# Kernel optimization log

Measured on AMD Instinct MI355X. Metric: run time of the kernel, lower is better.

Reference implementation:

```python
import jax, jax.numpy as jnp
import numpy as np

C = 1.0          # curvature
TOP_K = 5
LAMBDA_H = 0.01
TAU = 0.1        # forward default
NEG_SAMPLES = 20 # forward default
EPS = 1e-9
B, D = 4096, 64


def _to_ball(v):
    # map gaussian vectors strictly inside the unit Poincare ball
    return 0.8 * v / (1.0 + jnp.linalg.norm(v, axis=-1, keepdims=True))


def setup_inputs() -> dict:
    key = jax.random.key(0)
    ka, kt = jax.random.split(key)
    audio = _to_ball(jax.random.normal(ka, (B, D), dtype=jnp.float32))
    text = _to_ball(jax.random.normal(kt, (B, D), dtype=jnp.float32))
    return {"audio_embeds": audio, "text_embeds": text}


def _pairwise_poincare(x, y, c=C):
    # ||x-y||^2 via gemm instead of materializing [N,N,D] diff tensor
    x_sq = jnp.sum(x * x, axis=-1, keepdims=True)          # [N,1]
    y_sq = jnp.sum(y * y, axis=-1, keepdims=True).T        # [1,M]
    diff_sq = jnp.maximum(x_sq + y_sq - 2.0 * (x @ y.T), 0.0)
    x_cl = jnp.minimum(x_sq, 1.0 - EPS)
    y_cl = jnp.minimum(y_sq, 1.0 - EPS)
    denom = jnp.maximum((1.0 - x_cl) * (1.0 - y_cl), EPS)
    z = jnp.maximum(1.0 + 2.0 * diff_sq / denom, 1.0 + EPS)
    return jnp.arccosh(z) / jnp.sqrt(jnp.asarray(c, x.dtype))


def _topk_triplet(embeds, key):
    n = embeds.shape[0]
    dist = _pairwise_poincare(embeds, embeds)
    dist = dist.at[jnp.arange(n), jnp.arange(n)].set(jnp.inf)  # fill_diagonal_(inf)
    k = min(TOP_K, n - 1)
    neg_pos, pos_idx = jax.lax.top_k(-dist, k)                 # k smallest distances
    pos_term = jax.scipy.special.logsumexp(neg_pos / TAU, axis=1)  # logsumexp(-pos_dist/tau)
    # mask out top-k positives (diagonal stays in pool, holding +inf -> exp(-inf)=0)
    mask = jnp.ones((n, n), bool).at[jnp.arange(n)[:, None], pos_idx].set(False)
    # stable argsort: mask-True columns first, in original column order -> matches dist[i][mask[i]]
    order = jnp.argsort(jnp.where(mask, 0, 1), axis=1)
    pool = jnp.take_along_axis(dist, order[:, : n - k], axis=1)    # [n, n-k]
    samp = jax.random.randint(key, (n, NEG_SAMPLES), 0, n - k)
    neg_vals = jnp.take_along_axis(pool, samp, axis=1)             # [n, NEG_SAMPLES]
    neg_term = jax.scipy.special.logsumexp(-neg_vals / TAU, axis=1)
    return jnp.mean(neg_term - pos_term)  # mean of -(pos_term - neg_term)


def reference(audio_embeds, text_embeds):
    # HyperbolicLayeredLoss.forward returns lambda_h * (text_h + audio_h);
    # the cross-modal loss is computed but NOT added to the returned total in the source.
    key_text = jax.random.key(1)
    key_audio = jax.random.key(2)
    loss_text_h = _topk_triplet(text_embeds, key_text)
    loss_audio_h = _topk_triplet(audio_embeds, key_audio)
    return LAMBDA_H * (loss_text_h + loss_audio_h)
```

## Files before the change

kernel.cpp:

```cpp
#include <hip/hip_runtime.h>
#include <stdint.h>

#define JAX_PARTITIONABLE 1

constexpr int N = 4096;
constexpr int DIM = 64;
constexpr int TOPK = 5;
constexpr int NEGS = 20;
constexpr float TAU_ = 0.1f;
constexpr uint32_t SPAN = 4091u;
constexpr uint32_t MULT = 2309u;

constexpr int CQ = 256;
constexpr int NQ = N / CQ;
constexpr int NT = CQ / 16;
constexpr int RPB = 64;
constexpr int YSTRIDE = 136;

typedef __attribute__((ext_vector_type(8))) short bf16x8;
typedef __attribute__((ext_vector_type(4))) float f32x4;

__device__ __forceinline__ uint32_t rotl32(uint32_t v, int d) {
  return (v << d) | (v >> (32 - d));
}

__device__ __forceinline__ void threefry(uint32_t k0, uint32_t k1,
                                         uint32_t& x0, uint32_t& x1) {
  const uint32_t k2 = k0 ^ k1 ^ 0x1BD11BDAu;
  x0 += k0; x1 += k1;
#define TF_R(r) { x0 += x1; x1 = rotl32(x1, r); x1 ^= x0; }
  TF_R(13) TF_R(15) TF_R(26) TF_R(6)
  x0 += k1; x1 += k2 + 1u;
  TF_R(17) TF_R(29) TF_R(16) TF_R(24)
  x0 += k2; x1 += k0 + 2u;
  TF_R(13) TF_R(15) TF_R(26) TF_R(6)
  x0 += k0; x1 += k1 + 3u;
  TF_R(17) TF_R(29) TF_R(16) TF_R(24)
  x0 += k1; x1 += k2 + 4u;
  TF_R(13) TF_R(15) TF_R(26) TF_R(6)
  x0 += k2; x1 += k0 + 5u;
#undef TF_R
}

__device__ __forceinline__ uint32_t sample_idx(uint32_t seed, uint32_t f) {
#if JAX_PARTITIONABLE
  uint32_t a0 = 0u, a1 = 0u; threefry(0u, seed, a0, a1);
  uint32_t b0 = 0u, b1 = 1u; threefry(0u, seed, b0, b1);
  uint32_t h0 = 0u, h1 = f;  threefry(a0, a1, h0, h1);
  const uint32_t hi = h0 ^ h1;
  uint32_t l0 = 0u, l1 = f;  threefry(b0, b1, l0, l1);
  const uint32_t lo = l0 ^ l1;
#else
  uint32_t a0 = 0u, a1 = 2u; threefry(0u, seed, a0, a1);
  uint32_t c0 = 1u, c1 = 3u; threefry(0u, seed, c0, c1);
  const uint32_t HALF = (uint32_t)(N * NEGS / 2);
  uint32_t hi, lo;
  if (f < HALF) {
    uint32_t x0 = f, x1 = f + HALF; threefry(a0, c0, x0, x1); hi = x0;
    x0 = f; x1 = f + HALF;          threefry(a1, c1, x0, x1); lo = x0;
  } else {
    uint32_t x0 = f - HALF, x1 = f; threefry(a0, c0, x0, x1); hi = x1;
    x0 = f - HALF; x1 = f;          threefry(a1, c1, x0, x1); lo = x1;
  }
#endif
  return ((hi % SPAN) * MULT + (lo % SPAN)) % SPAN;
}

__device__ __forceinline__ float acosh_dev(float z) {
  return logf(z + sqrtf((z - 1.0f) * (z + 1.0f)));
}

__device__ __forceinline__ uint16_t f2bf(float f) {
  const uint32_t u = __float_as_uint(f);
  return (uint16_t)((u + 0x7FFFu + ((u >> 16) & 1u)) >> 16);
}
__device__ __forceinline__ float bf2f(uint16_t h) {
  return __uint_as_float((uint32_t)h << 16);
}

__global__ __launch_bounds__(64) void k_pre(const float* __restrict__ Xa,
                                            const float* __restrict__ Xt,
                                            uint16_t* __restrict__ Xs,
                                            float* __restrict__ ysq,
                                            float* __restrict__ inv) {
  const int m = blockIdx.y;
  const float* __restrict__ X = (m == 0) ? Xt : Xa;
  const int i = blockIdx.x * 64 + threadIdx.x;
  const float* xr = X + (size_t)i * DIM;

  uint32_t hb[DIM / 2], lb[DIM / 2];
  float s = 0.0f;
#pragma unroll
  for (int u = 0; u < DIM / 4; ++u) {
    const float4 v = *(const float4*)(xr + 4 * u);
    s = fmaf(v.x, v.x, s); s = fmaf(v.y, v.y, s);
    s = fmaf(v.z, v.z, s); s = fmaf(v.w, v.w, s);
    const uint16_t h0 = f2bf(v.x), h1 = f2bf(v.y), h2 = f2bf(v.z), h3 = f2bf(v.w);
    const uint16_t l0 = f2bf(v.x - bf2f(h0)), l1 = f2bf(v.y - bf2f(h1));
    const uint16_t l2 = f2bf(v.z - bf2f(h2)), l3 = f2bf(v.w - bf2f(h3));
    hb[2 * u]     = (uint32_t)h0 | ((uint32_t)h1 << 16);
    hb[2 * u + 1] = (uint32_t)h2 | ((uint32_t)h3 << 16);
    lb[2 * u]     = (uint32_t)l0 | ((uint32_t)l1 << 16);
    lb[2 * u + 1] = (uint32_t)l2 | ((uint32_t)l3 << 16);
  }
  uint32_t* dst = (uint32_t*)(Xs + (size_t)(m * N + i) * 128);
#pragma unroll
  for (int w = 0; w < 8; ++w) {
    uint4 qh = { hb[4 * w], hb[4 * w + 1], hb[4 * w + 2], hb[4 * w + 3] };
    ((uint4*)dst)[w] = qh;
  }
#pragma unroll
  for (int w = 0; w < 8; ++w) {
    uint4 ql = { lb[4 * w], lb[4 * w + 1], lb[4 * w + 2], lb[4 * w + 3] };
    ((uint4*)dst)[8 + w] = ql;
  }
  ysq[m * N + i] = s;
  inv[m * N + i] = 1.0f / (1.0f - fminf(s, 1.0f));
}

__global__ __launch_bounds__(256) void k_top5(
    const uint16_t* __restrict__ Xs, const float* __restrict__ ysq,
    const float* __restrict__ inv, uint64_t* __restrict__ partial) {
  const int lin = (int)blockIdx.x;
  const int wg = ((lin & 7) << 8) | (lin >> 3);
  const int m = wg >> 10;
  const int qq = (wg >> 6) & 15;
  const int rb = wg & 63;

  const int tid = (int)threadIdx.x;
  const int wid = tid >> 6;
  const int l = tid & 63;
  const int i0w = rb * RPB + wid * 16;
  const int j0q = qq * CQ;
  const int mN = m * N;
  const uint16_t* __restrict__ Xm = Xs + (size_t)m * N * 128;
  const int lc = l & 15;
  const int lk = l >> 4;
  const int lk4 = lk * 4;
  const int lk8 = lk * 8;
  const int sr = tid >> 4;
  const int sc8 = (tid & 15) * 8;

  __shared__ __align__(16) unsigned char smem[4 * 16 * YSTRIDE * 2 + 2048];
  uint16_t* ybuf = (uint16_t*)smem;
  float* sq_s = (float*)(smem + 4 * 16 * YSTRIDE * 2);
  float* iv_s = sq_s + CQ;

  bf16x8 xf[2][2];
#pragma unroll
  for (int c = 0; c < 2; ++c)
#pragma unroll
    for (int h = 0; h < 2; ++h)
      xf[c][h] = *(const bf16x8*)(Xm + (size_t)(i0w + lc) * 128 +
                                  h * 64 + c * 32 + lk8);

  const float xsq_i = ysq[mN + i0w + lc];
  const float inv2_i = 2.0f * inv[mN + i0w + lc];
  const int gi = i0w + lc;

  const uint64_t SENT = ((uint64_t)0x7F800000u << 32) | 0xFFFFFFFFu;
  uint64_t t5[TOPK];
#pragma unroll
  for (int t = 0; t < TOPK; ++t) t5[t] = SENT;
  float z5own = __uint_as_float(0x7F800000u);

  const f32x4 zz = {0.0f, 0.0f, 0.0f, 0.0f};
  const float INF_ = __uint_as_float(0x7F800000u);

  {
    if (tid < 64)
      *(float4*)&sq_s[tid * 4] = *(const float4*)&ysq[mN + j0q + tid * 4];
    else if (tid < 128)
      *(float4*)&iv_s[(tid - 64) * 4] =
          *(const float4*)&inv[mN + j0q + (tid - 64) * 4];
    *(uint4*)(ybuf + sr * YSTRIDE + sc8) =
        *(const uint4*)(Xm + (size_t)(j0q + sr) * 128 + sc8);
    *(uint4*)(ybuf + 16 * YSTRIDE + sr * YSTRIDE + sc8) =
        *(const uint4*)(Xm + (size_t)(j0q + 16 + sr) * 128 + sc8);
    __syncthreads();
  }

#define PROCESS(T, BUF)                                                        \
  {                                                                            \
    const uint16_t* yp = (BUF) + lc * YSTRIDE + lk8;                           \
    const bf16x8 Y0 = *(const bf16x8*)(yp);                                    \
    const bf16x8 Y1 = *(const bf16x8*)(yp + 32);                               \
    const bf16x8 Y2 = *(const bf16x8*)(yp + 64);                               \
    const bf16x8 Y3 = *(const bf16x8*)(yp + 96);                               \
    f32x4 acc;                \
    acc = __builtin_amdgcn_mfma_f32_16x16x32_bf16(Y0, xf[0][0], zz, 0, 0, 0);  \
    acc = __builtin_amdgcn_mfma_f32_16x16x32_bf16(Y1, xf[1][0], acc, 0, 0, 0); \
    acc = __builtin_amdgcn_mfma_f32_16x16x32_bf16(Y2, xf[0][0], acc, 0, 0, 0); \
    acc = __builtin_amdgcn_mfma_f32_16x16x32_bf16(Y3, xf[1][0], acc, 0, 0, 0); \
    acc = __builtin_amdgcn_mfma_f32_16x16x32_bf16(Y0, xf[0][1], acc, 0, 0, 0); \
    acc = __builtin_amdgcn_mfma_f32_16x16x32_bf16(Y1, xf[1][1], acc, 0, 0, 0); \
    const float4 sq4 = *(const float4*)&sq_s[(T) * 16 + lk4];                  \
    const float4 iv4 = *(const float4*)&iv_s[(T) * 16 + lk4];                  \
    const int jb = j0q + (T) * 16;                                             \
    float zt[4];                                                               \
    _Pragma("unroll") for (int p = 0; p < 4; ++p) {                            \
      const float yc = (p == 0) ? sq4.x : (p == 1) ? sq4.y                     \
                      : (p == 2) ? sq4.z : sq4.w;                              \
      const float ic = (p == 0) ? iv4.x : (p == 1) ? iv4.y                     \
                      : (p == 2) ? iv4.z : iv4.w;                              \
      const float diff = fmaxf(xsq_i + yc - 2.0f * acc[p], 0.0f);              \
      zt[p] = fmaf(diff * inv2_i, ic, 1.0f);                                   \
    }                                                                          \
    if (jb == i0w) {                           \
      _Pragma("unroll") for (int p = 0; p < 4; ++p)                            \
        if (gi == jb + lk4 + p) zt[p] = INF_;                                  \
    }                                                                          \
    const float zm = fminf(fminf(zt[0], zt[1]), fminf(zt[2], zt[3]));          \
    if (zm <= z5own) {                                                         \
      _Pragma("unroll") for (int p = 0; p < 4; ++p) {                          \
        uint64_t key = ((uint64_t)__float_as_uint(zt[p]) << 32) |              \
                       (uint32_t)(jb + lk4 + p);                               \
        if (key < t5[TOPK - 1]) {                                              \
          _Pragma("unroll") for (int tt = 0; tt < TOPK; ++tt) {                \
            const uint64_t cv = t5[tt];                                        \
            if (key < cv) { t5[tt] = key; key = cv; }                          \
          }                                                                    \
        }                                                                      \
      }                                                                        \
      z5own = __uint_as_float((uint32_t)(t5[TOPK - 1] >> 32));                 \
    }                                                                          \
  }

#pragma unroll 1
  for (int T = 0; T < NT; T += 2) {
    const bool hn = (T + 2 < NT);
    uint4 s2, s3;
    if (hn) {
      s2 = *(const uint4*)(Xm + (size_t)(j0q + (T + 2) * 16 + sr) * 128 + sc8);
      s3 = *(const uint4*)(Xm + (size_t)(j0q + (T + 3) * 16 + sr) * 128 + sc8);
    }
    PROCESS(T, ybuf + (size_t)((T) & 3) * 16 * YSTRIDE)
    PROCESS(T + 1, ybuf + (size_t)((T + 1) & 3) * 16 * YSTRIDE)
    if (hn) {
      *(uint4*)(ybuf + (size_t)((T + 2) & 3) * 16 * YSTRIDE + sr * YSTRIDE + sc8) = s2;
      *(uint4*)(ybuf + (size_t)((T + 3) & 3) * 16 * YSTRIDE + sr * YSTRIDE + sc8) = s3;
    }
    __syncthreads();
  }
#undef PROCESS

  uint64_t* mb = (uint64_t*)smem;
#pragma unroll
  for (int t = 0; t < TOPK; ++t)
    mb[((size_t)(wid * 16) + lc) * 21 + lk * TOPK + t] = t5[t];
  __syncthreads();

  if (l < 16) {
    uint64_t cur[TOPK];
#pragma unroll
    for (int t = 0; t < TOPK; ++t) cur[t] = mb[((size_t)(wid * 16) + l) * 21 + t];
    for (int c = 1; c < 4; ++c) {
      for (int t = 0; t < TOPK; ++t) {
        uint64_t key = mb[((size_t)(wid * 16) + l) * 21 + c * TOPK + t];
        if (key >= cur[TOPK - 1]) break;
#pragma unroll
        for (int u = 0; u < TOPK; ++u) {
          const uint64_t cv = cur[u];
          if (key < cv) { cur[u] = key; key = cv; }
        }
      }
    }
#pragma unroll
    for (int t = 0; t < TOPK; ++t)
      partial[((size_t)(m * NQ + qq) * N + i0w + l) * TOPK + t] = cur[t];
  }
}

__global__ __launch_bounds__(64) void k_neg(const float* __restrict__ Xa,
                                            const float* __restrict__ Xt,
                                            const float* __restrict__ ysq,
                                            const float* __restrict__ inv,
                                            const uint64_t* __restrict__ partial,
                                            float* __restrict__ rowres) {
  const int m = blockIdx.y;
  const int i = blockIdx.x;
  const float* __restrict__ X = (m == 0) ? Xt : Xa;
  const uint32_t seed = (m == 0) ? 1u : 2u;
  const int lane = threadIdx.x;

  __shared__ float4 xi4[DIM / 4];
  __shared__ float posv[TOPK];
  if (lane < DIM / 4) xi4[lane] = ((const float4*)(X + (size_t)i * DIM))[lane];
  __syncthreads();

  uint64_t cur[TOPK];
#pragma unroll
  for (int t = 0; t < TOPK; ++t)
    cur[t] = partial[((size_t)(m * NQ) * N + i) * TOPK + t];
  for (int q = 1; q < NQ; ++q) {
    for (int t = 0; t < TOPK; ++t) {
      uint64_t key = partial[((size_t)(m * NQ + q) * N + i) * TOPK + t];
      if (key >= cur[TOPK - 1]) break;
#pragma unroll
      for (int u = 0; u < TOPK; ++u) {
        const uint64_t cv = cur[u];
        if (key < cv) { cur[u] = key; key = cv; }
      }
    }
  }

  const float ysq_i = ysq[m * N + i];
  const float inv_i = inv[m * N + i];

  if (lane >= 32 && lane < 32 + TOPK) {
    const int t = lane - 32;
    const uint32_t c = (uint32_t)(cur[t] & 0xffffffffu);
    const float4* xc = (const float4*)(X + (size_t)c * DIM);
    float dot = 0.0f;
#pragma unroll
    for (int k = 0; k < DIM / 4; ++k) {
      const float4 a = xi4[k];
      const float4 b = xc[k];
      dot = fmaf(a.x, b.x, dot); dot = fmaf(a.y, b.y, dot);
      dot = fmaf(a.z, b.z, dot); dot = fmaf(a.w, b.w, dot);
    }
    const float diff = fmaxf(ysq_i + ysq[m * N + c] - 2.0f * dot, 0.0f);
    const float z = 1.0f + 2.0f * diff * inv_i * inv[m * N + c];
    posv[t] = -acosh_dev(z) / TAU_;
  }

  uint32_t pidx[TOPK];
#pragma unroll
  for (int t = 0; t < TOPK; ++t) pidx[t] = (uint32_t)(cur[t] & 0xffffffffu);

#define CSWAP(a, b)                                                           \
  { const uint32_t mn = pidx[a] < pidx[b] ? pidx[a] : pidx[b];                \
    const uint32_t mx = pidx[a] < pidx[b] ? pidx[b] : pidx[a];                \
    pidx[a] = mn; pidx[b] = mx; }
  CSWAP(0, 1) CSWAP(3, 4) CSWAP(2, 4) CSWAP(2, 3) CSWAP(1, 4)
  CSWAP(0, 3) CSWAP(0, 2) CSWAP(1, 3) CSWAP(1, 2)
#undef CSWAP

  float v = -1e30f;
  if (lane < NEGS) {
    const uint32_t f = (uint32_t)i * (uint32_t)NEGS + (uint32_t)lane;
    uint32_t c = sample_idx(seed, f);
#pragma unroll
    for (int t = 0; t < TOPK; ++t) c += (c >= pidx[t]) ? 1u : 0u;
    if (c != (uint32_t)i) {
      const float4* xc = (const float4*)(X + (size_t)c * DIM);
      float dot = 0.0f;
#pragma unroll
      for (int k = 0; k < DIM / 4; ++k) {
        const float4 a = xi4[k];
        const float4 b = xc[k];
        dot = fmaf(a.x, b.x, dot); dot = fmaf(a.y, b.y, dot);
        dot = fmaf(a.z, b.z, dot); dot = fmaf(a.w, b.w, dot);
      }
      const float diff = fmaxf(ysq_i + ysq[m * N + c] - 2.0f * dot, 0.0f);
      const float z = 1.0f + 2.0f * diff * inv_i * inv[m * N + c];
      v = -acosh_dev(z) / TAU_;
    }
  }

  __syncthreads();

  float vmax = v;
#pragma unroll
  for (int o = 32; o > 0; o >>= 1) vmax = fmaxf(vmax, __shfl_xor(vmax, o, 64));
  float e = expf(v - vmax);
  float ss = e;
#pragma unroll
  for (int o = 32; o > 0; o >>= 1) ss += __shfl_xor(ss, o, 64);

  if (lane == 0) {
    float vm = -1e30f;
#pragma unroll
    for (int t = 0; t < TOPK; ++t) vm = fmaxf(vm, posv[t]);
    float ps = 0.0f;
#pragma unroll
    for (int t = 0; t < TOPK; ++t) ps += expf(posv[t] - vm);
    const float pos = vm + logf(ps);
    rowres[m * N + i] = (vmax + logf(ss)) - pos;
  }
}

__global__ __launch_bounds__(256) void k_reduce(const float* __restrict__ rowres,
                                                float* __restrict__ out) {
  __shared__ double sh[256];
  double s = 0.0;
  for (int idx = threadIdx.x; idx < 2 * N; idx += 256) s += (double)rowres[idx];
  sh[threadIdx.x] = s;
  __syncthreads();
  for (int o = 128; o > 0; o >>= 1) {
    if (threadIdx.x < o) sh[threadIdx.x] += sh[threadIdx.x + o];
    __syncthreads();
  }
  if (threadIdx.x == 0) out[0] = (float)(0.01 * (sh[0] / (double)N));
}

extern "C" void kernel_launch(void* const* d_in, const int* in_sizes, int n_in,
                              void* d_out, int out_size, void* d_ws,
                              size_t ws_size, hipStream_t stream) {
  const float* Xa = (const float*)d_in[0];
  const float* Xt = (const float*)d_in[1];
  float* out = (float*)d_out;

  float* ysq = (float*)d_ws;
  float* inv = ysq + 2 * N;
  uint64_t* partial = (uint64_t*)(inv + 2 * N);
  float* rowres = (float*)(partial + (size_t)2 * NQ * N * TOPK);
  uint16_t* Xs = (uint16_t*)(rowres + 2 * N);

  k_pre<<<dim3(N / 64, 2), 64, 0, stream>>>(Xa, Xt, Xs, ysq, inv);
  k_top5<<<(N / RPB) * NQ * 2, 256, 0, stream>>>(Xs, ysq, inv, partial);
  k_neg<<<dim3(N, 2), 64, 0, stream>>>(Xa, Xt, ysq, inv, partial, rowres);
  k_reduce<<<1, 256, 0, stream>>>(rowres, out);
}
```

Measured before the change: 104.8 us.

## Split top-5 search into bound pass and filtered scan with candidate lists

The full top-5 pass over all 16 column chunks is replaced by two stages. A bound kernel computes a top-5 over 4 of the chunks, and a scan kernel goes over the other 12 chunks. The scan only appends keys that beat the 5th-best bound to a per-row list, using atomics, instead of keeping a sorted insertion per tile. k_neg then merges the partial results with the list. This cuts the in-loop top-5 maintenance and the partial traffic, but adds a launch, atomics, and a CAP=64 overflow risk that could drop true neighbours.

Result: faster. 100.1 us, median of 2 (-4.6%).

```diff
diff --git a/kernel.cpp b/kernel.cpp
--- a/kernel.cpp
+++ b/kernel.cpp
@@ -12,10 +12,11 @@
 constexpr uint32_t MULT = 2309u;
 
 constexpr int CQ = 256;
-constexpr int NQ = N / CQ;
 constexpr int NT = CQ / 16;
 constexpr int RPB = 64;
 constexpr int YSTRIDE = 136;
+constexpr int NQB = 4;
+constexpr int CAP = 64;
 
 typedef __attribute__((ext_vector_type(8))) short bf16x8;
 typedef __attribute__((ext_vector_type(4))) float f32x4;
@@ -82,7 +83,8 @@
                                             const float* __restrict__ Xt,
                                             uint16_t* __restrict__ Xs,
                                             float* __restrict__ ysq,
-                                            float* __restrict__ inv) {
+                                            float* __restrict__ inv,
+                                            uint32_t* __restrict__ cnt) {
   const int m = blockIdx.y;
   const float* __restrict__ X = (m == 0) ? Xt : Xa;
   const int i = blockIdx.x * 64 + threadIdx.x;
@@ -116,22 +118,22 @@
   }
   ysq[m * N + i] = s;
   inv[m * N + i] = 1.0f / (1.0f - fminf(s, 1.0f));
-}
-
-__global__ __launch_bounds__(256) void k_top5(
+  cnt[m * N + i] = 0u;
+}
+
+__global__ __launch_bounds__(256) void k_bound(
     const uint16_t* __restrict__ Xs, const float* __restrict__ ysq,
     const float* __restrict__ inv, uint64_t* __restrict__ partial) {
-  const int lin = (int)blockIdx.x;
-  const int wg = ((lin & 7) << 8) | (lin >> 3);
-  const int m = wg >> 10;
-  const int qq = (wg >> 6) & 15;
-  const int rb = wg & 63;
+  const int rb = (int)blockIdx.x;
+  const int qs = (int)blockIdx.y;
+  const int m = (int)blockIdx.z;
+  const int qr = rb >> 4;
+  const int j0q = (qr * NQB + qs) * CQ;
 
   const int tid = (int)threadIdx.x;
   const int wid = tid >> 6;
   const int l = tid & 63;
   const int i0w = rb * RPB + wid * 16;
-  const int j0q = qq * CQ;
   const int mN = m * N;
   const uint16_t* __restrict__ Xm = Xs + (size_t)m * N * 128;
   const int lc = l & 15;
@@ -206,7 +208,7 @@
       const float diff = fmaxf(xsq_i + yc - 2.0f * acc[p], 0.0f);              \
       zt[p] = fmaf(diff * inv2_i, ic, 1.0f);                                   \
     }                                                                          \
-    if (jb == i0w) {                           \
+    if (jb == i0w) {                                                           \
       _Pragma("unroll") for (int p = 0; p < 4; ++p)                            \
         if (gi == jb + lk4 + p) zt[p] = INF_;                                  \
     }                                                                          \
@@ -267,8 +269,140 @@
     }
 #pragma unroll
     for (int t = 0; t < TOPK; ++t)
-      partial[((size_t)(m * NQ + qq) * N + i0w + l) * TOPK + t] = cur[t];
-  }
+      partial[((size_t)(m * NQB + qs) * N + i0w + l) * TOPK + t] = cur[t];
+  }
+}
+
+__global__ __launch_bounds__(256) void k_scan(
+    const uint16_t* __restrict__ Xs, const float* __restrict__ ysq,
+    const float* __restrict__ inv, const uint64_t* __restrict__ partial,
+    uint32_t* __restrict__ cnt, uint64_t* __restrict__ rowlist) {
+  const int rb = (int)blockIdx.x;
+  const int s = (int)blockIdx.y;
+  const int m = (int)blockIdx.z;
+  const int qr = rb >> 4;
+  const int gs = (s < qr * NQB) ? s : s + NQB;
+  const int j0q = gs * CQ;
+
+  const int tid = (int)threadIdx.x;
+  const int wid = tid >> 6;
+  const int l = tid & 63;
+  const int i0w = rb * RPB + wid * 16;
+  const int mN = m * N;
+  const uint16_t* __restrict__ Xm = Xs + (size_t)m * N * 128;
+  const int lc = l & 15;
+  const int lk = l >> 4;
+  const int lk4 = lk * 4;
+  const int lk8 = lk * 8;
+  const int sr = tid >> 4;
+  const int sc8 = (tid & 15) * 8;
+  const int gi = i0w + lc;
+
+  __shared__ __align__(16) unsigned char smem[4 * 16 * YSTRIDE * 2 + 2048];
+  uint16_t* ybuf = (uint16_t*)smem;
+  float* sq_s = (float*)(smem + 4 * 16 * YSTRIDE * 2);
+  float* iv_s = sq_s + CQ;
+
+  bf16x8 xf[2][2];
+#pragma unroll
+  for (int c = 0; c < 2; ++c)
+#pragma unroll
+    for (int h = 0; h < 2; ++h)
+      xf[c][h] = *(const bf16x8*)(Xm + (size_t)gi * 128 + h * 64 + c * 32 + lk8);
+
+  const float xsq_i = ysq[mN + gi];
+  const float inv2_i = 2.0f * inv[mN + gi];
+
+  uint64_t b5[TOPK];
+#pragma unroll
+  for (int t = 0; t < TOPK; ++t)
+    b5[t] = partial[((size_t)(m * NQB) * N + gi) * TOPK + t];
+  for (int q = 1; q < NQB; ++q) {
+    for (int t = 0; t < TOPK; ++t) {
+      uint64_t key = partial[((size_t)(m * NQB + q) * N + gi) * TOPK + t];
+      if (key >= b5[TOPK - 1]) break;
+#pragma unroll
+      for (int u = 0; u < TOPK; ++u) {
+        const uint64_t cv = b5[u];
+        if (key < cv) { b5[u] = key; key = cv; }
+      }
+    }
+  }
+  const uint64_t bound = b5[TOPK - 1];
+  const float bz = __uint_as_float((uint32_t)(bound >> 32));
+
+  const f32x4 zz = {0.0f, 0.0f, 0.0f, 0.0f};
+
+  {
+    if (tid < 64)
+      *(float4*)&sq_s[tid * 4] = *(const float4*)&ysq[mN + j0q + tid * 4];
+    else if (tid < 128)
+      *(float4*)&iv_s[(tid - 64) * 4] =
+          *(const float4*)&inv[mN + j0q + (tid - 64) * 4];
+    *(uint4*)(ybuf + sr * YSTRIDE + sc8) =
+        *(const uint4*)(Xm + (size_t)(j0q + sr) * 128 + sc8);
+    *(uint4*)(ybuf + 16 * YSTRIDE + sr * YSTRIDE + sc8) =
+        *(const uint4*)(Xm + (size_t)(j0q + 16 + sr) * 128 + sc8);
+    __syncthreads();
+  }
+
+#define PSCAN(T, BUF)                                                          \
+  {                                                                            \
+    const uint16_t* yp = (BUF) + lc * YSTRIDE + lk8;                           \
+    const bf16x8 Y0 = *(const bf16x8*)(yp);                                    \
+    const bf16x8 Y1 = *(const bf16x8*)(yp + 32);                               \
+    const bf16x8 Y2 = *(const bf16x8*)(yp + 64);                               \
+    const bf16x8 Y3 = *(const bf16x8*)(yp + 96);                               \
+    f32x4 acc;                        \
+    acc = __builtin_amdgcn_mfma_f32_16x16x32_bf16(Y0, xf[0][0], zz, 0, 0, 0);  \
+    acc = __builtin_amdgcn_mfma_f32_16x16x32_bf16(Y1, xf[1][0], acc, 0, 0, 0); \
+    acc = __builtin_amdgcn_mfma_f32_16x16x32_bf16(Y2, xf[0][0], acc, 0, 0, 0); \
+    acc = __builtin_amdgcn_mfma_f32_16x16x32_bf16(Y3, xf[1][0], acc, 0, 0, 0); \
+    acc = __builtin_amdgcn_mfma_f32_16x16x32_bf16(Y0, xf[0][1], acc, 0, 0, 0); \
+    acc = __builtin_amdgcn_mfma_f32_16x16x32_bf16(Y1, xf[1][1], acc, 0, 0, 0); \
+    const float4 sq4 = *(const float4*)&sq_s[(T) * 16 + lk4];                  \
+    const float4 iv4 = *(const float4*)&iv_s[(T) * 16 + lk4];                  \
+    const int jb = j0q + (T) * 16;                                             \
+    float zt[4];                                                               \
+    _Pragma("unroll") for (int p = 0; p < 4; ++p) {                            \
+      const float yc = (p == 0) ? sq4.x : (p == 1) ? sq4.y                     \
+                      : (p == 2) ? sq4.z : sq4.w;                              \
+      const float ic = (p == 0) ? iv4.x : (p == 1) ? iv4.y                     \
+                      : (p == 2) ? iv4.z : iv4.w;                              \
+      const float diff = fmaxf(xsq_i + yc - 2.0f * acc[p], 0.0f);              \
+      zt[p] = fmaf(diff * inv2_i, ic, 1.0f);                                   \
+    }                                                                          \
+    const float zm = fminf(fminf(zt[0], zt[1]), fminf(zt[2], zt[3]));          \
+    if (zm <= bz) {                   \
+      _Pragma("unroll") for (int p = 0; p < 4; ++p) {                          \
+        const uint64_t key = ((uint64_t)__float_as_uint(zt[p]) << 32) |        \
+                             (uint32_t)(jb + lk4 + p);                         \
+        if (key < bound) {                                                     \
+          const uint32_t slot = atomicAdd(&cnt[mN + gi], 1u);                  \
+          if (slot < (uint32_t)CAP)                                            \
+            rowlist[(size_t)(mN + gi) * CAP + slot] = key;                     \
+        }                                                                      \
+      }                                                                        \
+    }                                                                          \
+  }
+
+#pragma unroll 1
+  for (int T = 0; T < NT; T += 2) {
+    const bool hn = (T + 2 < NT);
+    uint4 s2, s3;
+    if (hn) {
+      s2 = *(const uint4*)(Xm + (size_t)(j0q + (T + 2) * 16 + sr) * 128 + sc8);
+      s3 = *(const uint4*)(Xm + (size_t)(j0q + (T + 3) * 16 + sr) * 128 + sc8);
+    }
+    PSCAN(T, ybuf + (size_t)((T) & 3) * 16 * YSTRIDE)
+    PSCAN(T + 1, ybuf + (size_t)((T + 1) & 3) * 16 * YSTRIDE)
+    if (hn) {
+      *(uint4*)(ybuf + (size_t)((T + 2) & 3) * 16 * YSTRIDE + sr * YSTRIDE + sc8) = s2;
+      *(uint4*)(ybuf + (size_t)((T + 3) & 3) * 16 * YSTRIDE + sr * YSTRIDE + sc8) = s3;
+    }
+    __syncthreads();
+  }
+#undef PSCAN
 }
 
 __global__ __launch_bounds__(64) void k_neg(const float* __restrict__ Xa,
@@ -276,6 +410,8 @@
                                             const float* __restrict__ ysq,
                                             const float* __restrict__ inv,
                                             const uint64_t* __restrict__ partial,
+                                            const uint32_t* __restrict__ cnt,
+                                            const uint64_t* __restrict__ rowlist,
                                             float* __restrict__ rowres) {
   const int m = blockIdx.y;
   const int i = blockIdx.x;
@@ -291,15 +427,28 @@
   uint64_t cur[TOPK];
 #pragma unroll
   for (int t = 0; t < TOPK; ++t)
-    cur[t] = partial[((size_t)(m * NQ) * N + i) * TOPK + t];
-  for (int q = 1; q < NQ; ++q) {
+    cur[t] = partial[((size_t)(m * NQB) * N + i) * TOPK + t];
+  for (int q = 1; q < NQB; ++q) {
     for (int t = 0; t < TOPK; ++t) {
-      uint64_t key = partial[((size_t)(m * NQ + q) * N + i) * TOPK + t];
+      uint64_t key = partial[((size_t)(m * NQB + q) * N + i) * TOPK + t];
       if (key >= cur[TOPK - 1]) break;
 #pragma unroll
       for (int u = 0; u < TOPK; ++u) {
         const uint64_t cv = cur[u];
         if (key < cv) { cur[u] = key; key = cv; }
+      }
+    }
+  }
+  {
+    const uint32_t c_ = min(cnt[m * N + i], (uint32_t)CAP);
+    for (uint32_t sv = 0; sv < c_; ++sv) {
+      uint64_t key = rowlist[(size_t)(m * N + i) * CAP + sv];
+      if (key < cur[TOPK - 1]) {
+#pragma unroll
+        for (int u = 0; u < TOPK; ++u) {
+          const uint64_t cv = cur[u];
+          if (key < cv) { cur[u] = key; key = cv; }
+        }
       }
     }
   }
@@ -404,11 +553,16 @@
   float* ysq = (float*)d_ws;
   float* inv = ysq + 2 * N;
   uint64_t* partial = (uint64_t*)(inv + 2 * N);
-  float* rowres = (float*)(partial + (size_t)2 * NQ * N * TOPK);
-  uint16_t* Xs = (uint16_t*)(rowres + 2 * N);
-
-  k_pre<<<dim3(N / 64, 2), 64, 0, stream>>>(Xa, Xt, Xs, ysq, inv);
-  k_top5<<<(N / RPB) * NQ * 2, 256, 0, stream>>>(Xs, ysq, inv, partial);
-  k_neg<<<dim3(N, 2), 64, 0, stream>>>(Xa, Xt, ysq, inv, partial, rowres);
+  float* rowres = (float*)(partial + (size_t)2 * NQB * N * TOPK);
+  uint32_t* cnt = (uint32_t*)(rowres + 2 * N);
+  uint64_t* rowlist = (uint64_t*)(cnt + 2 * N);
+  uint16_t* Xs = (uint16_t*)(rowlist + (size_t)2 * N * CAP);
+
+  k_pre<<<dim3(N / 64, 2), 64, 0, stream>>>(Xa, Xt, Xs, ysq, inv, cnt);
+  k_bound<<<dim3(N / RPB, NQB, 2), 256, 0, stream>>>(Xs, ysq, inv, partial);
+  k_scan<<<dim3(N / RPB, 12, 2), 256, 0, stream>>>(Xs, ysq, inv, partial, cnt,
+                                                   rowlist);
+  k_neg<<<dim3(N, 2), 64, 0, stream>>>(Xa, Xt, ysq, inv, partial, cnt, rowlist,
+                                       rowres);
   k_reduce<<<1, 256, 0, stream>>>(rowres, out);
 }
```
